# Performance work log

Measured on AMD Instinct MI355X. Metric: run time of the kernel, lower is better.

## Reference

```python
import jax, jax.numpy as jnp
import numpy as np

LAMBDA_SOFTMAX = 9.0  # opt.lambda_softmax (smooth)
LAMBDA_LSE = 6.0      # opt.lambda_lse (LogSumExp aggregation)
EPS = 1e-8


def l2norm(x, axis, eps=EPS):
    # matches torch l2norm: x / (sqrt(sum(x^2)) + eps)
    return x / (jnp.sqrt(jnp.sum(x * x, axis=axis, keepdims=True)) + eps)


def setup_inputs() -> dict:
    key = jax.random.key(0)
    k1, k2 = jax.random.split(key)
    images = jax.random.normal(k1, (128, 36, 256), dtype=jnp.float32)    # (n_image, n_regions, d)
    captions = jax.random.normal(k2, (256, 48, 256), dtype=jnp.float32)  # (n_caption, max_n_word, d)
    return {"images": images, "captions": captions}


def reference(images, captions):
    """Vectorized SCAN xattn_score_t2i with raw_feature_norm='clipped_l2norm',
    agg_func='LogSumExp'. Returns (n_image, n_caption) similarity matrix.
    Axes: c=caption, i=image, r=region (sourceL), w=word (queryL), d=embed."""
    # func_attention: attn = bmm(context, query^T) -> (b, sourceL, queryL); here batched over (c, i)
    attn = jnp.einsum('ird,cwd->cirw', images, captions)       # [c,i,r,w]
    # first norm: LeakyReLU(0.1) then l2norm over queryL dim (torch dim=2 of (b,r,w))
    attn = jax.nn.leaky_relu(attn, negative_slope=0.1)
    attn = l2norm(attn, axis=3)
    # transpose to (b, queryL, sourceL) and smoothed softmax over sourceL
    attn = jnp.swapaxes(attn, 2, 3)                            # [c,i,w,r]
    attn = jax.nn.softmax(attn * LAMBDA_SOFTMAX, axis=-1)
    # weightedContext = attn @ context  -> (b, queryL, d)
    wctx = jnp.einsum('ciwr,ird->ciwd', attn, images)          # [c,i,w,d]
    # cosine similarity over d between expanded caption words and weighted context
    cap = captions[:, None, :, :]                              # [c,1,w,d]
    w12 = jnp.sum(cap * wctx, axis=-1)                         # [c,i,w]
    w1 = jnp.sqrt(jnp.sum(cap * cap, axis=-1))
    w2 = jnp.sqrt(jnp.sum(wctx * wctx, axis=-1))
    row_sim = w12 / jnp.maximum(w1 * w2, EPS)                  # [c,i,w]
    # LogSumExp aggregation over words: log(sum exp(s*lse)) / lse
    sim = jax.scipy.special.logsumexp(row_sim * LAMBDA_LSE, axis=-1) / LAMBDA_LSE  # [c,i]
    return sim.T                                               # (n_image, n_caption)
```

## Files before the change

### kernel.cpp

```cpp
#include <hip/hip_runtime.h>
#include <math.h>

#define NI 128
#define NC 256
#define NR 36
#define NW 48
#define ND 256

#define PIB 264
#define PG  72
#define PSP 52

#define SOFT_SCALE 12.984255368000671f
#define LSE_SCALE   8.656170245333781f

typedef __bf16 bf16;
typedef __bf16 bf16x8 __attribute__((ext_vector_type(8)));
typedef __bf16 bf16x4 __attribute__((ext_vector_type(4)));
typedef float  f32x4  __attribute__((ext_vector_type(4)));

#define OFF_IB    0
#define OFF_G     19008
#define OFF_P     24192
#define OFF_GUARD 30848
#define SMEM_TOTAL 30976

#define MFMA16(A,B,C) __builtin_amdgcn_mfma_f32_16x16x32_bf16(A, B, C, 0, 0, 0)

__device__ __forceinline__ float dpp_add16(float v) {
    int x = __builtin_bit_cast(int, v);
    v += __builtin_bit_cast(float, __builtin_amdgcn_update_dpp(0, x, 0xB1, 0xF, 0xF, true));
    x = __builtin_bit_cast(int, v);
    v += __builtin_bit_cast(float, __builtin_amdgcn_update_dpp(0, x, 0x4E, 0xF, 0xF, true));
    x = __builtin_bit_cast(int, v);
    v += __builtin_bit_cast(float, __builtin_amdgcn_update_dpp(0, x, 0x141, 0xF, 0xF, true));
    x = __builtin_bit_cast(int, v);
    v += __builtin_bit_cast(float, __builtin_amdgcn_update_dpp(0, x, 0x140, 0xF, 0xF, true));
    return v;
}

__device__ __forceinline__ float lrelu(float t) {
    return __builtin_fmaf(0.55f, t, 0.45f * __builtin_fabsf(t));
}

__global__ __launch_bounds__(256)
void prep_kernel(const float* __restrict__ captions, bf16* __restrict__ capb,
                 float* __restrict__ w1g)
{
    const int c = blockIdx.x >> 2, q = blockIdx.x & 3;
    const int wave = threadIdx.x >> 6, lane = threadIdx.x & 63;
    #pragma unroll
    for (int j = 0; j < 3; ++j) {
        int w = q * 12 + wave * 3 + j;
        size_t off = ((size_t)c * NW + w) * ND + lane * 4;
        float4 v = *(const float4*)(captions + off);
        bf16x4 h = { (bf16)v.x, (bf16)v.y, (bf16)v.z, (bf16)v.w };
        *(bf16x4*)(capb + off) = h;
        float s = v.x*v.x + v.y*v.y + v.z*v.z + v.w*v.w;
        s += __shfl_xor(s, 1);  s += __shfl_xor(s, 2);  s += __shfl_xor(s, 4);
        s += __shfl_xor(s, 8);  s += __shfl_xor(s, 16); s += __shfl_xor(s, 32);
        if (lane == 0) w1g[c * NW + w] = LSE_SCALE / sqrtf(s);
    }
}

__device__ __forceinline__ bf16x8 ld_cvt_f32(const float* p, float& ss) {
    float4 lo = *(const float4*)p;
    float4 hi = *(const float4*)(p + 4);
    ss += lo.x*lo.x + lo.y*lo.y + lo.z*lo.z + lo.w*lo.w
        + hi.x*hi.x + hi.y*hi.y + hi.z*hi.z + hi.w*hi.w;
    bf16x8 r = { (bf16)lo.x, (bf16)lo.y, (bf16)lo.z, (bf16)lo.w,
                 (bf16)hi.x, (bf16)hi.y, (bf16)hi.z, (bf16)hi.w };
    return r;
}

template<bool USE_WS>
__global__ __attribute__((amdgpu_flat_work_group_size(256, 256), amdgpu_waves_per_eu(4, 4)))
void scan_main(const float* __restrict__ images,
               const float* __restrict__ captions,
               const bf16* __restrict__ capb,
               const float* __restrict__ w1g,
               float* __restrict__ out)
{
    __shared__ __align__(16) unsigned char smem[SMEM_TOTAL];
    bf16* sIb = (bf16*)(smem + OFF_IB);
    bf16* sG  = (bf16*)(smem + OFF_G);

    const int tid  = threadIdx.x;
    const int wave = tid >> 6;
    const int lane = tid & 63;
    const int quad = lane >> 4;
    const int l15  = lane & 15;
    const int i    = blockIdx.x >> 4;
    const int c0   = (blockIdx.x & 15) * 16;

    bf16* sPw = (bf16*)(smem + OFF_P) + wave * (16 * PSP);

    const int rb2 = 20;

    const float* gI = images + (size_t)i * NR * ND;
    #pragma unroll
    for (int k = 0; k < 9; ++k) {
        int t = tid + k * 256;
        int e = t * 4, r = e >> 8, d = e & 255;
        float4 v = *(const float4*)(gI + e);
        bf16x4 h = { (bf16)v.x, (bf16)v.y, (bf16)v.z, (bf16)v.w };
        *(bf16x4*)&sIb[r * PIB + d] = h;
    }
    {
        uint32_t* pG = (uint32_t*)sG;
        #pragma unroll
        for (int k = 0; k < 6; ++k) { int x = tid + k * 256; if (x < 1296) pG[x] = 0u; }
        uint32_t* pP = (uint32_t*)(smem + OFF_P);
        #pragma unroll
        for (int k = 0; k < 7; ++k) { int x = tid + k * 256; if (x < 1696) pP[x] = 0u; }
    }
    __syncthreads();

    if (wave < 3) {
        const int mb = (wave == 2) ? rb2 : wave * 16;
        f32x4 g0 = {0,0,0,0}, g1 = {0,0,0,0}, g2 = {0,0,0,0};
        #pragma unroll
        for (int ks = 0; ks < 8; ++ks) {
            bf16x8 a  = *(const bf16x8*)&sIb[(mb + l15)  * PIB + ks * 32 + quad * 8];
            bf16x8 b0 = *(const bf16x8*)&sIb[(l15)       * PIB + ks * 32 + quad * 8];
            bf16x8 b1 = *(const bf16x8*)&sIb[(16 + l15)  * PIB + ks * 32 + quad * 8];
            bf16x8 b2 = *(const bf16x8*)&sIb[(rb2 + l15) * PIB + ks * 32 + quad * 8];
            g0 = MFMA16(a, b0, g0); g1 = MFMA16(a, b1, g1); g2 = MFMA16(a, b2, g2);
        }
        #pragma unroll
        for (int p = 0; p < 4; ++p) {
            int m = mb + quad * 4 + p;
            sG[m * PG + l15]       = (bf16)g0[p];
            sG[m * PG + 16 + l15]  = (bf16)g1[p];
            sG[m * PG + rb2 + l15] = (bf16)g2[p];
        }
    }
    __syncthreads();

    for (int it = 0; it < 4; ++it) {
        const int c = c0 + wave * 4 + it;

        f32x4 acc[3][3] = {};
        float ssc[3] = {0.f, 0.f, 0.f};
        float w1f[3][4];
        const bf16*  ab   = USE_WS ? capb + ((size_t)c * NW + l15) * ND + quad * 8 : nullptr;
        const float* ab32 = USE_WS ? nullptr : captions + ((size_t)c * NW + l15) * ND + quad * 8;
        #pragma unroll
        for (int ks = 0; ks < 8; ++ks) {
            bf16x8 a0, a1, a2;
            if (USE_WS) {
                a0 = *(const bf16x8*)(ab + ks * 32);
                a1 = *(const bf16x8*)(ab + 16 * ND + ks * 32);
                a2 = *(const bf16x8*)(ab + 32 * ND + ks * 32);
            } else {
                a0 = ld_cvt_f32(ab32 + ks * 32, ssc[0]);
                a1 = ld_cvt_f32(ab32 + 16 * ND + ks * 32, ssc[1]);
                a2 = ld_cvt_f32(ab32 + 32 * ND + ks * 32, ssc[2]);
            }
            bf16x8 b0 = *(const bf16x8*)&sIb[(l15)       * PIB + ks * 32 + quad * 8];
            bf16x8 b1 = *(const bf16x8*)&sIb[(16 + l15)  * PIB + ks * 32 + quad * 8];
            bf16x8 b2 = *(const bf16x8*)&sIb[(rb2 + l15) * PIB + ks * 32 + quad * 8];
            acc[0][0] = MFMA16(a0, b0, acc[0][0]);
            acc[1][0] = MFMA16(a1, b0, acc[1][0]);
            acc[2][0] = MFMA16(a2, b0, acc[2][0]);
            acc[0][1] = MFMA16(a0, b1, acc[0][1]);
            acc[1][1] = MFMA16(a1, b1, acc[1][1]);
            acc[2][1] = MFMA16(a2, b1, acc[2][1]);
            acc[0][2] = MFMA16(a0, b2, acc[0][2]);
            acc[1][2] = MFMA16(a1, b2, acc[1][2]);
            acc[2][2] = MFMA16(a2, b2, acc[2][2]);
        }
        if (!USE_WS) {
            #pragma unroll
            for (int mt = 0; mt < 3; ++mt) {
                float s = ssc[mt];
                s += __shfl_xor(s, 16); s += __shfl_xor(s, 32);
                ssc[mt] = LSE_SCALE * __frsqrt_rn(fmaxf(s, 1e-16f));
            }
            #pragma unroll
            for (int mt = 0; mt < 3; ++mt)
                #pragma unroll
                for (int p = 0; p < 4; ++p)
                    w1f[mt][p] = __shfl(ssc[mt], (lane & 48) + quad * 4 + p);
        }

        float c1[3], c2[3];
        #pragma unroll
        for (int nt = 0; nt < 3; ++nt) {
            float s = 0.f;
            #pragma unroll
            for (int mt = 0; mt < 3; ++mt)
                #pragma unroll
                for (int p = 0; p < 4; ++p) { float t = lrelu(acc[mt][nt][p]); s += t * t; }
            s += __shfl_xor(s, 16); s += __shfl_xor(s, 32);
            float inv = SOFT_SCALE * __frsqrt_rn(fmaxf(s, 1e-12f));
            c1[nt] = 0.55f * inv;
            c2[nt] = 0.45f * inv;
        }

        float esum = 0.f;
        #pragma unroll
        for (int mt = 0; mt < 3; ++mt) {
            float w1x[4];
            if (USE_WS) {
                #pragma unroll
                for (int p = 0; p < 4; ++p)
                    w1x[p] = w1g[(size_t)c * NW + mt * 16 + quad * 4 + p];
            } else {
                #pragma unroll
                for (int p = 0; p < 4; ++p) w1x[p] = w1f[mt][p];
            }
            float q0[4], q1[4], q2[4], w12v[4];
            #pragma unroll
            for (int p = 0; p < 4; ++p) {
                float a0v = acc[mt][0][p], a1v = acc[mt][1][p], a2v = acc[mt][2][p];
                float e0 = exp2f(__builtin_fmaf(c1[0], a0v, c2[0] * __builtin_fabsf(a0v)));
                float e1 = exp2f(__builtin_fmaf(c1[1], a1v, c2[1] * __builtin_fabsf(a1v)));
                float e2 = (l15 >= 12)
                    ? exp2f(__builtin_fmaf(c1[2], a2v, c2[2] * __builtin_fabsf(a2v)))
                    : 0.f;
                w12v[p] = dpp_add16(e0 * a0v + e1 * a1v + e2 * a2v);
                q0[p] = e0; q1[p] = e1; q2[p] = e2;
                int row = quad * 4 + p;
                sPw[row * PSP + l15]      = (bf16)e0;
                sPw[row * PSP + 16 + l15] = (bf16)e1;
                if (l15 >= 12) sPw[row * PSP + rb2 + l15] = (bf16)e2;
            }
            const bf16* ap = &sPw[l15 * PSP];
            bf16x8 pa0 = *(const bf16x8*)(ap + quad * 8);
            bf16x8 pa1 = *(const bf16x8*)(ap + 32 + quad * 8);
            f32x4 pg0 = {0,0,0,0}, pg1 = {0,0,0,0}, pg2 = {0,0,0,0};
            {
                bf16x8 t0 = *(const bf16x8*)&sG[(l15) * PG + quad * 8];
                bf16x8 t1 = *(const bf16x8*)&sG[(l15) * PG + 32 + quad * 8];
                pg0 = MFMA16(pa0, t0, pg0); pg0 = MFMA16(pa1, t1, pg0);
                bf16x8 t2 = *(const bf16x8*)&sG[(16 + l15) * PG + quad * 8];
                bf16x8 t3 = *(const bf16x8*)&sG[(16 + l15) * PG + 32 + quad * 8];
                pg1 = MFMA16(pa0, t2, pg1); pg1 = MFMA16(pa1, t3, pg1);
                bf16x8 t4 = *(const bf16x8*)&sG[(rb2 + l15) * PG + quad * 8];
                bf16x8 t5 = *(const bf16x8*)&sG[(rb2 + l15) * PG + 32 + quad * 8];
                pg2 = MFMA16(pa0, t4, pg2); pg2 = MFMA16(pa1, t5, pg2);
            }
            #pragma unroll
            for (int p = 0; p < 4; ++p) {
                float s2 = pg0[p] * q0[p] + pg1[p] * q1[p] + pg2[p] * q2[p];
                s2 = dpp_add16(s2);
                esum += exp2f(w12v[p] * __frsqrt_rn(fmaxf(s2, 1e-16f)) * w1x[p]);
            }
        }
        esum += __shfl_xor(esum, 16); esum += __shfl_xor(esum, 32);
        if (lane == 0) out[(size_t)i * NC + c] = logf(esum) * (1.0f / 6.0f);
    }
}

extern "C" void kernel_launch(void* const* d_in, const int* in_sizes, int n_in,
                              void* d_out, int out_size, void* d_ws, size_t ws_size,
                              hipStream_t stream) {
    const float* images   = (const float*)d_in[0];
    const float* captions = (const float*)d_in[1];
    float* out = (float*)d_out;

    const size_t need_w1  = (size_t)NC * NW * sizeof(float);
    const size_t need_cap = (size_t)NC * NW * ND * 2;
    bool use_ws = ws_size >= need_w1 + need_cap;

    dim3 grid(2048), block(256);
    if (use_ws) {
        float* w1g = (float*)d_ws;
        bf16*  capb = (bf16*)((char*)d_ws + need_w1);
        hipLaunchKernelGGL(prep_kernel, dim3(1024), dim3(256), 0, stream, captions, capb, w1g);
        hipLaunchKernelGGL((scan_main<true>), grid, block, 0, stream, images, captions, capb, w1g, out);
    } else {
        hipLaunchKernelGGL((scan_main<false>), grid, block, 0, stream, images, captions,
                           (const bf16*)nullptr, (const float*)nullptr, out);
    }
}
```

Before: 169.7 us.

## Software-pipeline next caption's QK MFMAs with current caption's softmax epilogue

In the workspace path, each wave now double-buffers its accumulators, computing the next caption's image-caption MFMA tiles in pieces interleaved with the current caption's exp/softmax and P·G MFMA epilogue. The intent is to hide global load latency and overlap MFMA with transcendental VALU work. The conditional e2 store is made branchless by writing to a dummy guard slot, and the DPP reduction of w12 is moved later. This doubles the accumulator registers, so the waves-per-EU lower bound is relaxed to 3, which risks lower occupancy or spills.

```diff
diff --git a/kernel.cpp b/kernel.cpp
--- a/kernel.cpp
+++ b/kernel.cpp
@@ -74,7 +74,7 @@
 }
 
 template<bool USE_WS>
-__global__ __attribute__((amdgpu_flat_work_group_size(256, 256), amdgpu_waves_per_eu(4, 4)))
+__global__ __attribute__((amdgpu_flat_work_group_size(256, 256), amdgpu_waves_per_eu(3, 4)))
 void scan_main(const float* __restrict__ images,
                const float* __restrict__ captions,
                const bf16* __restrict__ capb,
@@ -137,40 +137,142 @@
     }
     __syncthreads();
 
-    for (int it = 0; it < 4; ++it) {
-        const int c = c0 + wave * 4 + it;
-
-        f32x4 acc[3][3] = {};
-        float ssc[3] = {0.f, 0.f, 0.f};
-        float w1f[3][4];
-        const bf16*  ab   = USE_WS ? capb + ((size_t)c * NW + l15) * ND + quad * 8 : nullptr;
-        const float* ab32 = USE_WS ? nullptr : captions + ((size_t)c * NW + l15) * ND + quad * 8;
-        #pragma unroll
-        for (int ks = 0; ks < 8; ++ks) {
-            bf16x8 a0, a1, a2;
-            if (USE_WS) {
-                a0 = *(const bf16x8*)(ab + ks * 32);
-                a1 = *(const bf16x8*)(ab + 16 * ND + ks * 32);
-                a2 = *(const bf16x8*)(ab + 32 * ND + ks * 32);
-            } else {
-                a0 = ld_cvt_f32(ab32 + ks * 32, ssc[0]);
-                a1 = ld_cvt_f32(ab32 + 16 * ND + ks * 32, ssc[1]);
-                a2 = ld_cvt_f32(ab32 + 32 * ND + ks * 32, ssc[2]);
-            }
+    if constexpr (USE_WS) {
+        const size_t cstep = (size_t)NW * ND;
+        const bf16* ab0 = capb + ((size_t)(c0 + wave * 4) * NW + l15) * ND + quad * 8;
+        bf16* dumpp = (bf16*)(smem + OFF_GUARD) + lane;
+
+        auto qk_step = [&](f32x4 (&A)[3][3], const bf16* ab, int ks) {
+            bf16x8 a0 = *(const bf16x8*)(ab + ks * 32);
+            bf16x8 a1 = *(const bf16x8*)(ab + 16 * ND + ks * 32);
+            bf16x8 a2 = *(const bf16x8*)(ab + 32 * ND + ks * 32);
             bf16x8 b0 = *(const bf16x8*)&sIb[(l15)       * PIB + ks * 32 + quad * 8];
             bf16x8 b1 = *(const bf16x8*)&sIb[(16 + l15)  * PIB + ks * 32 + quad * 8];
             bf16x8 b2 = *(const bf16x8*)&sIb[(rb2 + l15) * PIB + ks * 32 + quad * 8];
-            acc[0][0] = MFMA16(a0, b0, acc[0][0]);
-            acc[1][0] = MFMA16(a1, b0, acc[1][0]);
-            acc[2][0] = MFMA16(a2, b0, acc[2][0]);
-            acc[0][1] = MFMA16(a0, b1, acc[0][1]);
-            acc[1][1] = MFMA16(a1, b1, acc[1][1]);
-            acc[2][1] = MFMA16(a2, b1, acc[2][1]);
-            acc[0][2] = MFMA16(a0, b2, acc[0][2]);
-            acc[1][2] = MFMA16(a1, b2, acc[1][2]);
-            acc[2][2] = MFMA16(a2, b2, acc[2][2]);
+            A[0][0] = MFMA16(a0, b0, A[0][0]);
+            A[1][0] = MFMA16(a1, b0, A[1][0]);
+            A[2][0] = MFMA16(a2, b0, A[2][0]);
+            A[0][1] = MFMA16(a0, b1, A[0][1]);
+            A[1][1] = MFMA16(a1, b1, A[1][1]);
+            A[2][1] = MFMA16(a2, b1, A[2][1]);
+            A[0][2] = MFMA16(a0, b2, A[0][2]);
+            A[1][2] = MFMA16(a1, b2, A[1][2]);
+            A[2][2] = MFMA16(a2, b2, A[2][2]);
+        };
+
+        f32x4 accP[3][3] = {}, accQ[3][3];
+        #pragma unroll
+        for (int ks = 0; ks < 8; ++ks) qk_step(accP, ab0, ks);
+
+        #pragma unroll
+        for (int it = 0; it < 4; ++it) {
+            f32x4 (&cur)[3][3] = (it & 1) ? accQ : accP;
+            f32x4 (&nxt)[3][3] = (it & 1) ? accP : accQ;
+            const bf16* abn = ab0 + (size_t)(it + 1) * cstep;
+            const int c = c0 + wave * 4 + it;
+
+            if (it < 3) {
+                #pragma unroll
+                for (int x = 0; x < 3; ++x)
+                    #pragma unroll
+                    for (int y = 0; y < 3; ++y) nxt[x][y] = (f32x4){0.f, 0.f, 0.f, 0.f};
+            }
+
+            float c1[3], c2[3];
+            #pragma unroll
+            for (int nt = 0; nt < 3; ++nt) {
+                float s = 0.f;
+                #pragma unroll
+                for (int mt = 0; mt < 3; ++mt)
+                    #pragma unroll
+                    for (int p = 0; p < 4; ++p) { float t = lrelu(cur[mt][nt][p]); s += t * t; }
+                s += __shfl_xor(s, 16); s += __shfl_xor(s, 32);
+                float inv = SOFT_SCALE * __frsqrt_rn(fmaxf(s, 1e-12f));
+                c1[nt] = 0.55f * inv;
+                c2[nt] = 0.45f * inv;
+            }
+
+            float esum = 0.f;
+            #pragma unroll
+            for (int mt = 0; mt < 3; ++mt) {
+                float w1x[4];
+                #pragma unroll
+                for (int p = 0; p < 4; ++p)
+                    w1x[p] = w1g[(size_t)c * NW + mt * 16 + quad * 4 + p];
+
+                float q0[4], q1[4], q2[4], w12r[4];
+                #pragma unroll
+                for (int p = 0; p < 4; ++p) {
+                    float a0v = cur[mt][0][p], a1v = cur[mt][1][p], a2v = cur[mt][2][p];
+                    float e0 = exp2f(__builtin_fmaf(c1[0], a0v, c2[0] * __builtin_fabsf(a0v)));
+                    float e1 = exp2f(__builtin_fmaf(c1[1], a1v, c2[1] * __builtin_fabsf(a1v)));
+                    float e2t = exp2f(__builtin_fmaf(c1[2], a2v, c2[2] * __builtin_fabsf(a2v)));
+                    float e2 = (l15 >= 12) ? e2t : 0.f;
+                    w12r[p] = e0 * a0v + e1 * a1v + e2 * a2v;
+                    q0[p] = e0; q1[p] = e1; q2[p] = e2;
+                    int row = quad * 4 + p;
+                    sPw[row * PSP + l15]      = (bf16)e0;
+                    sPw[row * PSP + 16 + l15] = (bf16)e1;
+                    bf16* d2 = (l15 >= 12) ? &sPw[row * PSP + rb2 + l15] : dumpp;
+                    *d2 = (bf16)e2;
+                }
+
+                if (it < 3) { qk_step(nxt, abn, mt * 2); qk_step(nxt, abn, mt * 2 + 1); }
+
+                const bf16* ap = &sPw[l15 * PSP];
+                bf16x8 pa0 = *(const bf16x8*)(ap + quad * 8);
+                bf16x8 pa1 = *(const bf16x8*)(ap + 32 + quad * 8);
+                f32x4 pg0 = {0,0,0,0}, pg1 = {0,0,0,0}, pg2 = {0,0,0,0};
+                {
+                    bf16x8 t0 = *(const bf16x8*)&sG[(l15) * PG + quad * 8];
+                    bf16x8 t1 = *(const bf16x8*)&sG[(l15) * PG + 32 + quad * 8];
+                    pg0 = MFMA16(pa0, t0, pg0); pg0 = MFMA16(pa1, t1, pg0);
+                    bf16x8 t2 = *(const bf16x8*)&sG[(16 + l15) * PG + quad * 8];
+                    bf16x8 t3 = *(const bf16x8*)&sG[(16 + l15) * PG + 32 + quad * 8];
+                    pg1 = MFMA16(pa0, t2, pg1); pg1 = MFMA16(pa1, t3, pg1);
+                    bf16x8 t4 = *(const bf16x8*)&sG[(rb2 + l15) * PG + quad * 8];
+                    bf16x8 t5 = *(const bf16x8*)&sG[(rb2 + l15) * PG + 32 + quad * 8];
+                    pg2 = MFMA16(pa0, t4, pg2); pg2 = MFMA16(pa1, t5, pg2);
+                }
+
+                if (it < 3 && mt == 2) { qk_step(nxt, abn, 6); qk_step(nxt, abn, 7); }
+
+                #pragma unroll
+                for (int p = 0; p < 4; ++p) {
+                    float s2 = pg0[p] * q0[p] + pg1[p] * q1[p] + pg2[p] * q2[p];
+                    s2 = dpp_add16(s2);
+                    float w12 = dpp_add16(w12r[p]);
+                    esum += exp2f(w12 * __frsqrt_rn(fmaxf(s2, 1e-16f)) * w1x[p]);
+                }
+            }
+            esum += __shfl_xor(esum, 16); esum += __shfl_xor(esum, 32);
+            if (lane == 0) out[(size_t)i * NC + c] = logf(esum) * (1.0f / 6.0f);
         }
-        if (!USE_WS) {
+    } else {
+        for (int it = 0; it < 4; ++it) {
+            const int c = c0 + wave * 4 + it;
+            f32x4 acc[3][3] = {};
+            float ssc[3] = {0.f, 0.f, 0.f};
+            float w1f[3][4];
+            const float* ab32 = captions + ((size_t)c * NW + l15) * ND + quad * 8;
+            #pragma unroll
+            for (int ks = 0; ks < 8; ++ks) {
+                bf16x8 a0 = ld_cvt_f32(ab32 + ks * 32, ssc[0]);
+                bf16x8 a1 = ld_cvt_f32(ab32 + 16 * ND + ks * 32, ssc[1]);
+                bf16x8 a2 = ld_cvt_f32(ab32 + 32 * ND + ks * 32, ssc[2]);
+                bf16x8 b0 = *(const bf16x8*)&sIb[(l15)       * PIB + ks * 32 + quad * 8];
+                bf16x8 b1 = *(const bf16x8*)&sIb[(16 + l15)  * PIB + ks * 32 + quad * 8];
+                bf16x8 b2 = *(const bf16x8*)&sIb[(rb2 + l15) * PIB + ks * 32 + quad * 8];
+                acc[0][0] = MFMA16(a0, b0, acc[0][0]);
+                acc[1][0] = MFMA16(a1, b0, acc[1][0]);
+                acc[2][0] = MFMA16(a2, b0, acc[2][0]);
+                acc[0][1] = MFMA16(a0, b1, acc[0][1]);
+                acc[1][1] = MFMA16(a1, b1, acc[1][1]);
+                acc[2][1] = MFMA16(a2, b1, acc[2][1]);
+                acc[0][2] = MFMA16(a0, b2, acc[0][2]);
+                acc[1][2] = MFMA16(a1, b2, acc[1][2]);
+                acc[2][2] = MFMA16(a2, b2, acc[2][2]);
+            }
             #pragma unroll
             for (int mt = 0; mt < 3; ++mt) {
                 float s = ssc[mt];
@@ -182,74 +284,64 @@
                 #pragma unroll
                 for (int p = 0; p < 4; ++p)
                     w1f[mt][p] = __shfl(ssc[mt], (lane & 48) + quad * 4 + p);
+
+            float c1[3], c2[3];
+            #pragma unroll
+            for (int nt = 0; nt < 3; ++nt) {
+                float s = 0.f;
+                #pragma unroll
+                for (int mt = 0; mt < 3; ++mt)
+                    #pragma unroll
+                    for (int p = 0; p < 4; ++p) { float t = lrelu(acc[mt][nt][p]); s += t * t; }
+                s += __shfl_xor(s, 16); s += __shfl_xor(s, 32);
+                float inv = SOFT_SCALE * __frsqrt_rn(fmaxf(s, 1e-12f));
+                c1[nt] = 0.55f * inv; c2[nt] = 0.45f * inv;
+            }
+
+            float esum = 0.f;
+            #pragma unroll
+            for (int mt = 0; mt < 3; ++mt) {
+                float q0[4], q1[4], q2[4], w12v[4];
+                #pragma unroll
+                for (int p = 0; p < 4; ++p) {
+                    float a0v = acc[mt][0][p], a1v = acc[mt][1][p], a2v = acc[mt][2][p];
+                    float e0 = exp2f(__builtin_fmaf(c1[0], a0v, c2[0] * __builtin_fabsf(a0v)));
+                    float e1 = exp2f(__builtin_fmaf(c1[1], a1v, c2[1] * __builtin_fabsf(a1v)));
+                    float e2 = (l15 >= 12)
+                        ? exp2f(__builtin_fmaf(c1[2], a2v, c2[2] * __builtin_fabsf(a2v)))
+                        : 0.f;
+                    w12v[p] = dpp_add16(e0 * a0v + e1 * a1v + e2 * a2v);
+                    q0[p] = e0; q1[p] = e1; q2[p] = e2;
+                    int row = quad * 4 + p;
+                    sPw[row * PSP + l15]      = (bf16)e0;
+                    sPw[row * PSP + 16 + l15] = (bf16)e1;
+                    if (l15 >= 12) sPw[row * PSP + rb2 + l15] = (bf16)e2;
+                }
+                const bf16* ap = &sPw[l15 * PSP];
+                bf16x8 pa0 = *(const bf16x8*)(ap + quad * 8);
+                bf16x8 pa1 = *(const bf16x8*)(ap + 32 + quad * 8);
+                f32x4 pg0 = {0,0,0,0}, pg1 = {0,0,0,0}, pg2 = {0,0,0,0};
+                {
+                    bf16x8 t0 = *(const bf16x8*)&sG[(l15) * PG + quad * 8];
+                    bf16x8 t1 = *(const bf16x8*)&sG[(l15) * PG + 32 + quad * 8];
+                    pg0 = MFMA16(pa0, t0, pg0); pg0 = MFMA16(pa1, t1, pg0);
+                    bf16x8 t2 = *(const bf16x8*)&sG[(16 + l15) * PG + quad * 8];
+                    bf16x8 t3 = *(const bf16x8*)&sG[(16 + l15) * PG + 32 + quad * 8];
+                    pg1 = MFMA16(pa0, t2, pg1); pg1 = MFMA16(pa1, t3, pg1);
+                    bf16x8 t4 = *(const bf16x8*)&sG[(rb2 + l15) * PG + quad * 8];
+                    bf16x8 t5 = *(const bf16x8*)&sG[(rb2 + l15) * PG + 32 + quad * 8];
+                    pg2 = MFMA16(pa0, t4, pg2); pg2 = MFMA16(pa1, t5, pg2);
+                }
+                #pragma unroll
+                for (int p = 0; p < 4; ++p) {
+                    float s2 = pg0[p] * q0[p] + pg1[p] * q1[p] + pg2[p] * q2[p];
+                    s2 = dpp_add16(s2);
+                    esum += exp2f(w12v[p] * __frsqrt_rn(fmaxf(s2, 1e-16f)) * w1f[mt][p]);
+                }
+            }
+            esum += __shfl_xor(esum, 16); esum += __shfl_xor(esum, 32);
+            if (lane == 0) out[(size_t)i * NC + c] = logf(esum) * (1.0f / 6.0f);
         }
-
-        float c1[3], c2[3];
-        #pragma unroll
-        for (int nt = 0; nt < 3; ++nt) {
-            float s = 0.f;
-            #pragma unroll
-            for (int mt = 0; mt < 3; ++mt)
-                #pragma unroll
-                for (int p = 0; p < 4; ++p) { float t = lrelu(acc[mt][nt][p]); s += t * t; }
-            s += __shfl_xor(s, 16); s += __shfl_xor(s, 32);
-            float inv = SOFT_SCALE * __frsqrt_rn(fmaxf(s, 1e-12f));
-            c1[nt] = 0.55f * inv;
-            c2[nt] = 0.45f * inv;
-        }
-
-        float esum = 0.f;
-        #pragma unroll
-        for (int mt = 0; mt < 3; ++mt) {
-            float w1x[4];
-            if (USE_WS) {
-                #pragma unroll
-                for (int p = 0; p < 4; ++p)
-                    w1x[p] = w1g[(size_t)c * NW + mt * 16 + quad * 4 + p];
-            } else {
-                #pragma unroll
-                for (int p = 0; p < 4; ++p) w1x[p] = w1f[mt][p];
-            }
-            float q0[4], q1[4], q2[4], w12v[4];
-            #pragma unroll
-            for (int p = 0; p < 4; ++p) {
-                float a0v = acc[mt][0][p], a1v = acc[mt][1][p], a2v = acc[mt][2][p];
-                float e0 = exp2f(__builtin_fmaf(c1[0], a0v, c2[0] * __builtin_fabsf(a0v)));
-                float e1 = exp2f(__builtin_fmaf(c1[1], a1v, c2[1] * __builtin_fabsf(a1v)));
-                float e2 = (l15 >= 12)
-                    ? exp2f(__builtin_fmaf(c1[2], a2v, c2[2] * __builtin_fabsf(a2v)))
-                    : 0.f;
-                w12v[p] = dpp_add16(e0 * a0v + e1 * a1v + e2 * a2v);
-                q0[p] = e0; q1[p] = e1; q2[p] = e2;
-                int row = quad * 4 + p;
-                sPw[row * PSP + l15]      = (bf16)e0;
-                sPw[row * PSP + 16 + l15] = (bf16)e1;
-                if (l15 >= 12) sPw[row * PSP + rb2 + l15] = (bf16)e2;
-            }
-            const bf16* ap = &sPw[l15 * PSP];
-            bf16x8 pa0 = *(const bf16x8*)(ap + quad * 8);
-            bf16x8 pa1 = *(const bf16x8*)(ap + 32 + quad * 8);
-            f32x4 pg0 = {0,0,0,0}, pg1 = {0,0,0,0}, pg2 = {0,0,0,0};
-            {
-                bf16x8 t0 = *(const bf16x8*)&sG[(l15) * PG + quad * 8];
-                bf16x8 t1 = *(const bf16x8*)&sG[(l15) * PG + 32 + quad * 8];
-                pg0 = MFMA16(pa0, t0, pg0); pg0 = MFMA16(pa1, t1, pg0);
-                bf16x8 t2 = *(const bf16x8*)&sG[(16 + l15) * PG + quad * 8];
-                bf16x8 t3 = *(const bf16x8*)&sG[(16 + l15) * PG + 32 + quad * 8];
-                pg1 = MFMA16(pa0, t2, pg1); pg1 = MFMA16(pa1, t3, pg1);
-                bf16x8 t4 = *(const bf16x8*)&sG[(rb2 + l15) * PG + quad * 8];
-                bf16x8 t5 = *(const bf16x8*)&sG[(rb2 + l15) * PG + 32 + quad * 8];
-                pg2 = MFMA16(pa0, t4, pg2); pg2 = MFMA16(pa1, t5, pg2);
-            }
-            #pragma unroll
-            for (int p = 0; p < 4; ++p) {
-                float s2 = pg0[p] * q0[p] + pg1[p] * q1[p] + pg2[p] * q2[p];
-                s2 = dpp_add16(s2);
-                esum += exp2f(w12v[p] * __frsqrt_rn(fmaxf(s2, 1e-16f)) * w1x[p]);
-            }
-        }
-        esum += __shfl_xor(esum, 16); esum += __shfl_xor(esum, 32);
-        if (lane == 0) out[(size_t)i * NC + c] = logf(esum) * (1.0f / 6.0f);
     }
 }
 
```

New measurement: 170.8 us. No clear change (+0.7%).

## Split softmax-exp and P·G phases across all word tiles with per-wave larger P buffer

Applied to the files above, without the earlier changes.

Restructures the per-caption epilogue into two phases: first compute all exponentials for the three word tiles and write them to a per-wave LDS buffer three times larger, then run the P·G MFMAs and final reductions. Hoists the w1 loads to vectorised float4 loads issued before the caption GEMM. It also makes the conditional e2 store branchless by redirecting it to a dummy slot. The aim is more independent work and fewer LDS round-trip stalls between the exp and MFMA stages. The cost is higher LDS use and more live registers, with waves_per_eu relaxed to 3–4 to allow this, which may lower occupancy.

```diff
diff --git a/kernel.cpp b/kernel.cpp
--- a/kernel.cpp
+++ b/kernel.cpp
@@ -22,8 +22,8 @@
 #define OFF_IB    0
 #define OFF_G     19008
 #define OFF_P     24192
-#define OFF_GUARD 30848
-#define SMEM_TOTAL 30976
+#define OFF_GUARD 44160
+#define SMEM_TOTAL 44288
 
 #define MFMA16(A,B,C) __builtin_amdgcn_mfma_f32_16x16x32_bf16(A, B, C, 0, 0, 0)
 
@@ -74,7 +74,7 @@
 }
 
 template<bool USE_WS>
-__global__ __attribute__((amdgpu_flat_work_group_size(256, 256), amdgpu_waves_per_eu(4, 4)))
+__global__ __attribute__((amdgpu_flat_work_group_size(256, 256), amdgpu_waves_per_eu(3, 4)))
 void scan_main(const float* __restrict__ images,
                const float* __restrict__ captions,
                const bf16* __restrict__ capb,
@@ -93,7 +93,7 @@
     const int i    = blockIdx.x >> 4;
     const int c0   = (blockIdx.x & 15) * 16;
 
-    bf16* sPw = (bf16*)(smem + OFF_P) + wave * (16 * PSP);
+    bf16* sPw = (bf16*)(smem + OFF_P) + wave * (48 * PSP);
 
     const int rb2 = 20;
 
@@ -112,7 +112,7 @@
         for (int k = 0; k < 6; ++k) { int x = tid + k * 256; if (x < 1296) pG[x] = 0u; }
         uint32_t* pP = (uint32_t*)(smem + OFF_P);
         #pragma unroll
-        for (int k = 0; k < 7; ++k) { int x = tid + k * 256; if (x < 1696) pP[x] = 0u; }
+        for (int k = 0; k < 20; ++k) { int x = tid + k * 256; if (x < 5024) pP[x] = 0u; }
     }
     __syncthreads();
 
@@ -137,12 +137,20 @@
     }
     __syncthreads();
 
+    bf16* dumpp = (bf16*)(smem + OFF_GUARD) + lane;
+
     for (int it = 0; it < 4; ++it) {
         const int c = c0 + wave * 4 + it;
 
+        float4 w1x[3];
+        if (USE_WS) {
+            #pragma unroll
+            for (int mt = 0; mt < 3; ++mt)
+                w1x[mt] = *(const float4*)&w1g[(size_t)c * NW + mt * 16 + quad * 4];
+        }
+
         f32x4 acc[3][3] = {};
         float ssc[3] = {0.f, 0.f, 0.f};
-        float w1f[3][4];
         const bf16*  ab   = USE_WS ? capb + ((size_t)c * NW + l15) * ND + quad * 8 : nullptr;
         const float* ab32 = USE_WS ? nullptr : captions + ((size_t)c * NW + l15) * ND + quad * 8;
         #pragma unroll
@@ -170,6 +178,7 @@
             acc[1][2] = MFMA16(a1, b2, acc[1][2]);
             acc[2][2] = MFMA16(a2, b2, acc[2][2]);
         }
+        float w1f[3][4];
         if (!USE_WS) {
             #pragma unroll
             for (int mt = 0; mt < 3; ++mt) {
@@ -198,35 +207,30 @@
             c2[nt] = 0.45f * inv;
         }
 
-        float esum = 0.f;
+        float q0[3][4], q1[3][4], q2[3][4], w12r[3][4];
         #pragma unroll
         for (int mt = 0; mt < 3; ++mt) {
-            float w1x[4];
-            if (USE_WS) {
-                #pragma unroll
-                for (int p = 0; p < 4; ++p)
-                    w1x[p] = w1g[(size_t)c * NW + mt * 16 + quad * 4 + p];
-            } else {
-                #pragma unroll
-                for (int p = 0; p < 4; ++p) w1x[p] = w1f[mt][p];
-            }
-            float q0[4], q1[4], q2[4], w12v[4];
             #pragma unroll
             for (int p = 0; p < 4; ++p) {
                 float a0v = acc[mt][0][p], a1v = acc[mt][1][p], a2v = acc[mt][2][p];
                 float e0 = exp2f(__builtin_fmaf(c1[0], a0v, c2[0] * __builtin_fabsf(a0v)));
                 float e1 = exp2f(__builtin_fmaf(c1[1], a1v, c2[1] * __builtin_fabsf(a1v)));
-                float e2 = (l15 >= 12)
-                    ? exp2f(__builtin_fmaf(c1[2], a2v, c2[2] * __builtin_fabsf(a2v)))
-                    : 0.f;
-                w12v[p] = dpp_add16(e0 * a0v + e1 * a1v + e2 * a2v);
-                q0[p] = e0; q1[p] = e1; q2[p] = e2;
-                int row = quad * 4 + p;
+                float e2t = exp2f(__builtin_fmaf(c1[2], a2v, c2[2] * __builtin_fabsf(a2v)));
+                float e2 = (l15 >= 12) ? e2t : 0.f;
+                w12r[mt][p] = e0 * a0v + e1 * a1v + e2 * a2v;
+                q0[mt][p] = e0; q1[mt][p] = e1; q2[mt][p] = e2;
+                int row = mt * 16 + quad * 4 + p;
                 sPw[row * PSP + l15]      = (bf16)e0;
                 sPw[row * PSP + 16 + l15] = (bf16)e1;
-                if (l15 >= 12) sPw[row * PSP + rb2 + l15] = (bf16)e2;
-            }
-            const bf16* ap = &sPw[l15 * PSP];
+                bf16* d2 = (l15 >= 12) ? &sPw[row * PSP + rb2 + l15] : dumpp;
+                *d2 = (bf16)e2;
+            }
+        }
+
+        float esum = 0.f;
+        #pragma unroll
+        for (int mt = 0; mt < 3; ++mt) {
+            const bf16* ap = &sPw[(mt * 16 + l15) * PSP];
             bf16x8 pa0 = *(const bf16x8*)(ap + quad * 8);
             bf16x8 pa1 = *(const bf16x8*)(ap + 32 + quad * 8);
             f32x4 pg0 = {0,0,0,0}, pg1 = {0,0,0,0}, pg2 = {0,0,0,0};
@@ -243,9 +247,11 @@
             }
             #pragma unroll
             for (int p = 0; p < 4; ++p) {
-                float s2 = pg0[p] * q0[p] + pg1[p] * q1[p] + pg2[p] * q2[p];
+                float s2 = pg0[p] * q0[mt][p] + pg1[p] * q1[mt][p] + pg2[p] * q2[mt][p];
                 s2 = dpp_add16(s2);
-                esum += exp2f(w12v[p] * __frsqrt_rn(fmaxf(s2, 1e-16f)) * w1x[p]);
+                float w12 = dpp_add16(w12r[mt][p]);
+                float wf = USE_WS ? ((const float*)&w1x[mt])[p] : w1f[mt][p];
+                esum += exp2f(w12 * __frsqrt_rn(fmaxf(s2, 1e-16f)) * wf);
             }
         }
         esum += __shfl_xor(esum, 16); esum += __shfl_xor(esum, 32);
```

New measurement: 175.9 us. 1.04x slower.

## Double-buffer softmax probability staging to overlap exp and MFMA stages

Applied to the files above, without the earlier changes.

Splits the per-m-tile softmax into a write stage (exp, store to LDS) and a read stage (MFMA against the Gram matrix, final exp). Two per-wave LDS buffers let the stages interleave, so the exp work of one tile can overlap the LDS round trip and MFMAs of another. It also reuses the acc registers for the exp values, loads w1 as a float4, and relaxes waves_per_eu to 4..8. LDS use per block grows, which may affect occupancy, and the interleaving depends on the compiler scheduling across the reused buffer.

```diff
diff --git a/kernel.cpp b/kernel.cpp
--- a/kernel.cpp
+++ b/kernel.cpp
@@ -22,8 +22,8 @@
 #define OFF_IB    0
 #define OFF_G     19008
 #define OFF_P     24192
-#define OFF_GUARD 30848
-#define SMEM_TOTAL 30976
+#define OFF_GUARD 37504
+#define SMEM_TOTAL 37632
 
 #define MFMA16(A,B,C) __builtin_amdgcn_mfma_f32_16x16x32_bf16(A, B, C, 0, 0, 0)
 
@@ -73,8 +73,56 @@
     return r;
 }
 
+#define STAGE_W(MT, BUF, W12) do {                                                      \
+    _Pragma("unroll")                                                                   \
+    for (int p = 0; p < 4; ++p) {                                                       \
+        float a0v = acc[MT][0][p], a1v = acc[MT][1][p], a2v = acc[MT][2][p];            \
+        float e0 = exp2f(__builtin_fmaf(c1[0], a0v, c2[0] * __builtin_fabsf(a0v)));     \
+        float e1 = exp2f(__builtin_fmaf(c1[1], a1v, c2[1] * __builtin_fabsf(a1v)));     \
+        float e2 = (l15 >= 12)                                                          \
+            ? exp2f(__builtin_fmaf(c1[2], a2v, c2[2] * __builtin_fabsf(a2v)))           \
+            : 0.f;                                                   \
+        W12[p] = e0 * a0v + e1 * a1v + e2 * a2v;                                        \
+        acc[MT][0][p] = e0; acc[MT][1][p] = e1; acc[MT][2][p] = e2;       \
+        int row = quad * 4 + p;                                                         \
+        (BUF)[row * PSP + l15]      = (bf16)e0;                                         \
+        (BUF)[row * PSP + 16 + l15] = (bf16)e1;                                         \
+        if (l15 >= 12) (BUF)[row * PSP + rb2 + l15] = (bf16)e2;        \
+    }                                                                                   \
+} while (0)
+
+#define STAGE_R(MT, BUF, W12) do {                                                      \
+    const bf16* ap = (BUF) + l15 * PSP;                                                 \
+    bf16x8 pa0 = *(const bf16x8*)(ap + quad * 8);                                       \
+    bf16x8 pa1 = *(const bf16x8*)(ap + 32 + quad * 8);  \
+    f32x4 pg0 = {0,0,0,0}, pg1 = {0,0,0,0}, pg2 = {0,0,0,0};                            \
+    {                                                                                   \
+        bf16x8 t0 = *(const bf16x8*)&sG[(l15) * PG + quad * 8];                         \
+        bf16x8 t1 = *(const bf16x8*)&sG[(l15) * PG + 32 + quad * 8];                    \
+        pg0 = MFMA16(pa0, t0, pg0); pg0 = MFMA16(pa1, t1, pg0);                         \
+        bf16x8 t2 = *(const bf16x8*)&sG[(16 + l15) * PG + quad * 8];                    \
+        bf16x8 t3 = *(const bf16x8*)&sG[(16 + l15) * PG + 32 + quad * 8];               \
+        pg1 = MFMA16(pa0, t2, pg1); pg1 = MFMA16(pa1, t3, pg1);                         \
+        bf16x8 t4 = *(const bf16x8*)&sG[(rb2 + l15) * PG + quad * 8];                   \
+        bf16x8 t5 = *(const bf16x8*)&sG[(rb2 + l15) * PG + 32 + quad * 8];              \
+        pg2 = MFMA16(pa0, t4, pg2); pg2 = MFMA16(pa1, t5, pg2);                         \
+    }                                                                                   \
+    float4 wq = {0.f, 0.f, 0.f, 0.f};                                                   \
+    if constexpr (USE_WS)                                                               \
+        wq = *(const float4*)&w1g[(size_t)c * NW + (MT) * 16 + quad * 4];               \
+    _Pragma("unroll")                                                                   \
+    for (int p = 0; p < 4; ++p) {                                                       \
+        float s2 = pg0[p] * acc[MT][0][p] + pg1[p] * acc[MT][1][p]                      \
+                 + pg2[p] * acc[MT][2][p];                       \
+        s2 = dpp_add16(s2);                                                             \
+        float w12 = dpp_add16(W12[p]);                                                  \
+        float wf = USE_WS ? ((const float*)&wq)[p] : w1f[MT][p];                        \
+        esum += exp2f(w12 * __frsqrt_rn(fmaxf(s2, 1e-16f)) * wf);                       \
+    }                                                                                   \
+} while (0)
+
 template<bool USE_WS>
-__global__ __attribute__((amdgpu_flat_work_group_size(256, 256), amdgpu_waves_per_eu(4, 4)))
+__global__ __attribute__((amdgpu_flat_work_group_size(256, 256), amdgpu_waves_per_eu(4, 8)))
 void scan_main(const float* __restrict__ images,
                const float* __restrict__ captions,
                const bf16* __restrict__ capb,
@@ -93,7 +141,8 @@
     const int i    = blockIdx.x >> 4;
     const int c0   = (blockIdx.x & 15) * 16;
 
-    bf16* sPw = (bf16*)(smem + OFF_P) + wave * (16 * PSP);
+    bf16* bufA = (bf16*)(smem + OFF_P) + wave * (32 * PSP);
+    bf16* bufB = bufA + 16 * PSP;
 
     const int rb2 = 20;
 
@@ -112,7 +161,7 @@
         for (int k = 0; k < 6; ++k) { int x = tid + k * 256; if (x < 1296) pG[x] = 0u; }
         uint32_t* pP = (uint32_t*)(smem + OFF_P);
         #pragma unroll
-        for (int k = 0; k < 7; ++k) { int x = tid + k * 256; if (x < 1696) pP[x] = 0u; }
+        for (int k = 0; k < 14; ++k) { int x = tid + k * 256; if (x < 3360) pP[x] = 0u; }
     }
     __syncthreads();
 
@@ -142,7 +191,7 @@
 
         f32x4 acc[3][3] = {};
         float ssc[3] = {0.f, 0.f, 0.f};
-        float w1f[3][4];
+        float w1f[3][4] = {};
         const bf16*  ab   = USE_WS ? capb + ((size_t)c * NW + l15) * ND + quad * 8 : nullptr;
         const float* ab32 = USE_WS ? nullptr : captions + ((size_t)c * NW + l15) * ND + quad * 8;
         #pragma unroll
@@ -199,55 +248,14 @@
         }
 
         float esum = 0.f;
-        #pragma unroll
-        for (int mt = 0; mt < 3; ++mt) {
-            float w1x[4];
-            if (USE_WS) {
-                #pragma unroll
-                for (int p = 0; p < 4; ++p)
-                    w1x[p] = w1g[(size_t)c * NW + mt * 16 + quad * 4 + p];
-            } else {
-                #pragma unroll
-                for (int p = 0; p < 4; ++p) w1x[p] = w1f[mt][p];
-            }
-            float q0[4], q1[4], q2[4], w12v[4];
-            #pragma unroll
-            for (int p = 0; p < 4; ++p) {
-                float a0v = acc[mt][0][p], a1v = acc[mt][1][p], a2v = acc[mt][2][p];
-                float e0 = exp2f(__builtin_fmaf(c1[0], a0v, c2[0] * __builtin_fabsf(a0v)));
-                float e1 = exp2f(__builtin_fmaf(c1[1], a1v, c2[1] * __builtin_fabsf(a1v)));
-                float e2 = (l15 >= 12)
-                    ? exp2f(__builtin_fmaf(c1[2], a2v, c2[2] * __builtin_fabsf(a2v)))
-                    : 0.f;
-                w12v[p] = dpp_add16(e0 * a0v + e1 * a1v + e2 * a2v);
-                q0[p] = e0; q1[p] = e1; q2[p] = e2;
-                int row = quad * 4 + p;
-                sPw[row * PSP + l15]      = (bf16)e0;
-                sPw[row * PSP + 16 + l15] = (bf16)e1;
-                if (l15 >= 12) sPw[row * PSP + rb2 + l15] = (bf16)e2;
-            }
-            const bf16* ap = &sPw[l15 * PSP];
-            bf16x8 pa0 = *(const bf16x8*)(ap + quad * 8);
-            bf16x8 pa1 = *(const bf16x8*)(ap + 32 + quad * 8);
-            f32x4 pg0 = {0,0,0,0}, pg1 = {0,0,0,0}, pg2 = {0,0,0,0};
-            {
-                bf16x8 t0 = *(const bf16x8*)&sG[(l15) * PG + quad * 8];
-                bf16x8 t1 = *(const bf16x8*)&sG[(l15) * PG + 32 + quad * 8];
-                pg0 = MFMA16(pa0, t0, pg0); pg0 = MFMA16(pa1, t1, pg0);
-                bf16x8 t2 = *(const bf16x8*)&sG[(16 + l15) * PG + quad * 8];
-                bf16x8 t3 = *(const bf16x8*)&sG[(16 + l15) * PG + 32 + quad * 8];
-                pg1 = MFMA16(pa0, t2, pg1); pg1 = MFMA16(pa1, t3, pg1);
-                bf16x8 t4 = *(const bf16x8*)&sG[(rb2 + l15) * PG + quad * 8];
-                bf16x8 t5 = *(const bf16x8*)&sG[(rb2 + l15) * PG + 32 + quad * 8];
-                pg2 = MFMA16(pa0, t4, pg2); pg2 = MFMA16(pa1, t5, pg2);
-            }
-            #pragma unroll
-            for (int p = 0; p < 4; ++p) {
-                float s2 = pg0[p] * q0[p] + pg1[p] * q1[p] + pg2[p] * q2[p];
-                s2 = dpp_add16(s2);
-                esum += exp2f(w12v[p] * __frsqrt_rn(fmaxf(s2, 1e-16f)) * w1x[p]);
-            }
-        }
+        float w12a[4], w12b[4], w12c[4];
+        STAGE_W(0, bufA, w12a);
+        STAGE_W(1, bufB, w12b);
+        STAGE_R(0, bufA, w12a);
+        STAGE_W(2, bufA, w12c);
+        STAGE_R(1, bufB, w12b);
+        STAGE_R(2, bufA, w12c);
+
         esum += __shfl_xor(esum, 16); esum += __shfl_xor(esum, 32);
         if (lane == 0) out[(size_t)i * NC + c] = logf(esum) * (1.0f / 6.0f);
     }
```

New measurement: 164.6 us. 3.0% less time.
